# Performance work log

Hardware: AMD Instinct MI355X
Metric: run time of the kernel (lower is better)

The kernel has to match this reference:

```python
import math
import jax, jax.numpy as jnp
import numpy as np

N_EXPERTS = 8
CAPACITY_FACTOR = 1.25
AUX_COEF = 0.01  # forward passes aux_loss_coef to BOTH z-loss and lb-loss


def setup_inputs() -> dict:
    key = jax.random.key(0)
    k1, k2 = jax.random.split(key)
    B, T, D = 4, 4096, 2048
    x = jax.random.normal(k1, (B, T, D), dtype=jnp.float32)
    # nn.Linear(d_model, n_experts, bias=False) weight: (n_experts, d_model)
    W = jax.random.normal(k2, (N_EXPERTS, D), dtype=jnp.float32) * (1.0 / math.sqrt(D))
    return {"x": x, "W": W}


def reference(x, W):
    B, T, D = x.shape
    S = B * T
    E = W.shape[0]
    capacity = int(math.ceil(S / E * CAPACITY_FACTOR))  # static

    x_flat = x.reshape(S, D)
    logits = jnp.einsum("sd,ed->se", x_flat, W)          # (S, E)
    probs = jax.nn.softmax(logits, axis=-1)               # (S, E)
    gate_vals = jnp.max(probs, axis=-1)                   # (S,)
    expert_idx = jnp.argmax(probs, axis=-1)               # (S,) int

    # rank of each token within its expert's queue (token order), 0-based
    onehot = jax.nn.one_hot(expert_idx, E, dtype=jnp.int32)        # (S, E)
    rank = jnp.sum(jnp.cumsum(onehot, axis=0) * onehot, axis=-1) - 1  # (S,)
    keep = rank < capacity
    kept_gates = jnp.where(keep, gate_vals, jnp.zeros((), gate_vals.dtype))

    # z-loss: coef * mean(logsumexp(logits)^2)
    log_z = jax.scipy.special.logsumexp(logits, axis=-1)
    z_loss = AUX_COEF * jnp.mean(log_z * log_z)

    # load-balance loss: coef * E * sum(f_i * p_i)
    p = jnp.mean(probs, axis=0)                                     # (E,)
    counts = jnp.zeros((E,), dtype=probs.dtype).at[expert_idx].add(1.0)
    f = counts / S
    lb_loss = AUX_COEF * E * jnp.sum(f * p)

    aux_loss = z_loss + lb_loss
    return expert_idx, kept_gates, aux_loss
```

## Files before the change

### kernel.cpp

```cpp
#include <hip/hip_runtime.h>

#define S_TOKENS 16384
#define DMODEL   2048
#define NE       8
#define CAPACITY 2560


__global__ __launch_bounds__(512) void logits_kernel(
    const float* __restrict__ x, const float* __restrict__ W,
    int* __restrict__ idx_out, float* __restrict__ gate_out,
    float* __restrict__ partials) {
    __shared__ float Ws[NE][DMODEL];
    __shared__ float sacc[16];

    const int tid  = threadIdx.x;
    const int wave = tid >> 6;
    const int lane = tid & 63;

    if (tid < 16) sacc[tid] = 0.0f;
    {
        const float4* __restrict__ Wg = (const float4*)W;
        float4* Wl = (float4*)Ws;
        #pragma unroll
        for (int i = 0; i < 8; ++i) Wl[i*512 + tid] = Wg[i*512 + tid];
    }
    __syncthreads();

    const int token0 = blockIdx.x * 32 + wave * 4;
    const float4* __restrict__ x0 = (const float4*)(x + (size_t)token0 * DMODEL);
    const float4* __restrict__ x1 = x0 + 512;
    const float4* __restrict__ x2 = x0 + 1024;
    const float4* __restrict__ x3 = x0 + 1536;

    float a0[NE], a1[NE], a2[NE], a3[NE];
    #pragma unroll
    for (int e = 0; e < NE; ++e) { a0[e]=0; a1[e]=0; a2[e]=0; a3[e]=0; }

    #pragma unroll
    for (int i = 0; i < 8; ++i) {
        const int j4 = i*64 + lane;
        float4 xv0 = x0[j4];
        float4 xv1 = x1[j4];
        float4 xv2 = x2[j4];
        float4 xv3 = x3[j4];
        #pragma unroll
        for (int e = 0; e < NE; ++e) {
            float4 w = ((const float4*)Ws[e])[j4];
            a0[e] += xv0.x*w.x + xv0.y*w.y + xv0.z*w.z + xv0.w*w.w;
            a1[e] += xv1.x*w.x + xv1.y*w.y + xv1.z*w.z + xv1.w*w.w;
            a2[e] += xv2.x*w.x + xv2.y*w.y + xv2.z*w.z + xv2.w*w.w;
            a3[e] += xv3.x*w.x + xv3.y*w.y + xv3.z*w.z + xv3.w*w.w;
        }
    }

    const bool hiHalf = (lane & 32) != 0;
    const bool oddQ   = (lane & 16) != 0;
    float lg[NE];
    #pragma unroll
    for (int e = 0; e < NE; ++e) {
        float s0 = a0[e] + __shfl_xor(a0[e], 32);
        float s1 = a1[e] + __shfl_xor(a1[e], 32);
        float s2 = a2[e] + __shfl_xor(a2[e], 32);
        float s3 = a3[e] + __shfl_xor(a3[e], 32);
        float u = hiHalf ? s2 : s0;
        float v = hiHalf ? s3 : s1;
        u += __shfl_xor(u, 16);
        v += __shfl_xor(v, 16);
        float r = oddQ ? v : u;
        r += __shfl_xor(r, 8);
        r += __shfl_xor(r, 4);
        r += __shfl_xor(r, 2);
        r += __shfl_xor(r, 1);
        lg[e] = r;
    }

    const int token = token0 + (lane >> 4);
    const int sub   = lane & 15;

    float m = lg[0]; int e = 0;
    #pragma unroll
    for (int k = 1; k < NE; ++k) { if (lg[k] > m) { m = lg[k]; e = k; } }
    float z = 0.0f;
    #pragma unroll
    for (int k = 0; k < NE; ++k) z += expf(lg[k] - m);
    float gate = 1.0f / z;
    float lz   = m + logf(z);

    if (sub == 0) {
        idx_out[token]  = e;
        gate_out[token] = gate;
        atomicAdd(&sacc[8], lz * lz);
    }
    if (sub < NE) {
        float b0 = (sub & 1) ? lg[1] : lg[0];
        float b1 = (sub & 1) ? lg[3] : lg[2];
        float b2 = (sub & 1) ? lg[5] : lg[4];
        float b3 = (sub & 1) ? lg[7] : lg[6];
        float c0 = (sub & 2) ? b1 : b0;
        float c1 = (sub & 2) ? b3 : b2;
        float ae = (sub & 4) ? c1 : c0;
        atomicAdd(&sacc[sub], expf(ae - m) * gate);
    }

    __syncthreads();
    if (tid < 9) partials[tid*512 + blockIdx.x] = sacc[tid];
}

__global__ __launch_bounds__(512, 1) void finalize_kernel(
    const int* __restrict__ idx, const float* __restrict__ gate,
    const float* __restrict__ partials, float* __restrict__ out) {
    __shared__ float facc[9];
    __shared__ int   cnt[256][9];
    const int t    = threadIdx.x;
    const int wv   = t >> 6;
    const int lane = t & 63;

    if (t < 9) facc[t] = 0.0f;
    __syncthreads();

    #pragma unroll
    for (int q = 0; q < 9; ++q) {
        float v = partials[q*512 + t];
        #pragma unroll
        for (int off = 32; off > 0; off >>= 1) v += __shfl_xor(v, off);
        if (lane == 0) atomicAdd(&facc[q], v);
    }

    const int spanBeg = wv * 32, spanEnd = spanBeg + 32;
    {
        int e = idx[spanBeg*64 + lane];
        for (int s = spanBeg; s < spanEnd; ++s) {
            int en = (s+1 < spanEnd) ? idx[(s+1)*64 + lane] : 0;
            #pragma unroll
            for (int q = 0; q < NE; ++q) {
                unsigned long long mk = __ballot(e == q);
                if (lane == q) cnt[s][q] = (int)__popcll(mk);
            }
            e = en;
        }
    }
    __syncthreads();

    int myc[NE];
    if (t < 256) {
        #pragma unroll
        for (int q = 0; q < NE; ++q) myc[q] = cnt[t][q];
    }
    for (int off = 1; off < 256; off <<= 1) {
        int v[NE];
        if (t < 256) {
            #pragma unroll
            for (int q = 0; q < NE; ++q) v[q] = (t >= off) ? cnt[t-off][q] : 0;
        }
        __syncthreads();
        if (t < 256) {
            #pragma unroll
            for (int q = 0; q < NE; ++q) cnt[t][q] += v[q];
        }
        __syncthreads();
    }

    if (t == 0) {
        float lb = 0.0f;
        #pragma unroll
        for (int q = 0; q < NE; ++q) {
            float f = (float)cnt[255][q] * (1.0f/S_TOKENS);
            float p = facc[q] * (1.0f/S_TOKENS);
            lb += f * p;
        }
        out[2*S_TOKENS] = 0.01f * (facc[8] * (1.0f/S_TOKENS)) + 0.08f * lb;
    }
    __syncthreads();
    if (t < 256) {
        #pragma unroll
        for (int q = 0; q < NE; ++q) cnt[t][q] -= myc[q];
    }
    __syncthreads();

    {
        int   e = idx[spanBeg*64 + lane];
        float g = gate[spanBeg*64 + lane];
        for (int s = spanBeg; s < spanEnd; ++s) {
            int   en = (s+1 < spanEnd) ? idx[(s+1)*64 + lane]  : 0;
            float gn = (s+1 < spanEnd) ? gate[(s+1)*64 + lane] : 0.0f;
            unsigned long long mym = 0;
            #pragma unroll
            for (int q = 0; q < NE; ++q) {
                unsigned long long mk = __ballot(e == q);
                if (e == q) mym = mk;
            }
            unsigned long long lt = (1ull << lane) - 1ull;
            int rank = cnt[s][e] + (int)__popcll(mym & lt);
            int token = s*64 + lane;
            out[token] = (float)e;
            out[S_TOKENS + token] = (rank < CAPACITY) ? g : 0.0f;
            e = en; g = gn;
        }
    }
}

extern "C" void kernel_launch(void* const* d_in, const int* in_sizes, int n_in,
                              void* d_out, int out_size, void* d_ws, size_t ws_size,
                              hipStream_t stream) {
    const float* x = (const float*)d_in[0];
    const float* W = (const float*)d_in[1];
    float* out = (float*)d_out;

    int*   ws_idx  = (int*)d_ws;
    float* ws_gate = (float*)d_ws + 16384;
    float* ws_part = (float*)d_ws + 32768;

    logits_kernel<<<512, 512, 0, stream>>>(x, W, ws_idx, ws_gate, ws_part);
    finalize_kernel<<<1, 512, 0, stream>>>(ws_idx, ws_gate, ws_part, out);
}
```

Measured before the change: 235.5 us.

## Split single-block finalize into scan kernel and parallel per-block output kernel

The single-block finalize, which both built per-chunk expert counts and wrote every token's output serially, is split in two. A 1024-thread scan kernel now computes the exclusive prefix counts per 64-token chunk and the aux loss. A 256-block output kernel then computes ranks and writes outputs in parallel. The logits kernel also changes its main loop from full unroll to unroll 2, to ease register pressure. This adds one extra kernel launch and a global round-trip for the prefix table.

```diff
diff --git a/kernel.cpp b/kernel.cpp
--- a/kernel.cpp
+++ b/kernel.cpp
@@ -10,8 +10,8 @@
     const float* __restrict__ x, const float* __restrict__ W,
     int* __restrict__ idx_out, float* __restrict__ gate_out,
     float* __restrict__ partials) {
-    __shared__ float Ws[NE][DMODEL];
-    __shared__ float sacc[16];
+    __shared__ float4 Ws4[NE][DMODEL/4];
+    __shared__ float  sacc[16];
 
     const int tid  = threadIdx.x;
     const int wave = tid >> 6;
@@ -20,7 +20,7 @@
     if (tid < 16) sacc[tid] = 0.0f;
     {
         const float4* __restrict__ Wg = (const float4*)W;
-        float4* Wl = (float4*)Ws;
+        float4* Wl = (float4*)Ws4;
         #pragma unroll
         for (int i = 0; i < 8; ++i) Wl[i*512 + tid] = Wg[i*512 + tid];
     }
@@ -36,7 +36,7 @@
     #pragma unroll
     for (int e = 0; e < NE; ++e) { a0[e]=0; a1[e]=0; a2[e]=0; a3[e]=0; }
 
-    #pragma unroll
+    #pragma unroll 2
     for (int i = 0; i < 8; ++i) {
         const int j4 = i*64 + lane;
         float4 xv0 = x0[j4];
@@ -45,7 +45,7 @@
         float4 xv3 = x3[j4];
         #pragma unroll
         for (int e = 0; e < NE; ++e) {
-            float4 w = ((const float4*)Ws[e])[j4];
+            float4 w = Ws4[e][j4];
             a0[e] += xv0.x*w.x + xv0.y*w.y + xv0.z*w.z + xv0.w*w.w;
             a1[e] += xv1.x*w.x + xv1.y*w.y + xv1.z*w.z + xv1.w*w.w;
             a2[e] += xv2.x*w.x + xv2.y*w.y + xv2.z*w.z + xv2.w*w.w;
@@ -106,9 +106,9 @@
     if (tid < 9) partials[tid*512 + blockIdx.x] = sacc[tid];
 }
 
-__global__ __launch_bounds__(512, 1) void finalize_kernel(
-    const int* __restrict__ idx, const float* __restrict__ gate,
-    const float* __restrict__ partials, float* __restrict__ out) {
+__global__ __launch_bounds__(1024) void scan_kernel(
+    const int* __restrict__ idx, const float* __restrict__ partials,
+    int* __restrict__ prefix, float* __restrict__ aux_out) {
     __shared__ float facc[9];
     __shared__ int   cnt[256][9];
     const int t    = threadIdx.x;
@@ -118,25 +118,28 @@
     if (t < 9) facc[t] = 0.0f;
     __syncthreads();
 
-    #pragma unroll
-    for (int q = 0; q < 9; ++q) {
-        float v = partials[q*512 + t];
-        #pragma unroll
-        for (int off = 32; off > 0; off >>= 1) v += __shfl_xor(v, off);
-        if (lane == 0) atomicAdd(&facc[q], v);
-    }
-
-    const int spanBeg = wv * 32, spanEnd = spanBeg + 32;
+    if (t < 512) {
+        #pragma unroll
+        for (int q = 0; q < 9; ++q) {
+            float v = partials[q*512 + t];
+            #pragma unroll
+            for (int off = 32; off > 0; off >>= 1) v += __shfl_xor(v, off);
+            if (lane == 0) atomicAdd(&facc[q], v);
+        }
+    }
+
     {
-        int e = idx[spanBeg*64 + lane];
-        for (int s = spanBeg; s < spanEnd; ++s) {
-            int en = (s+1 < spanEnd) ? idx[(s+1)*64 + lane] : 0;
+        const int s0 = wv * 16;
+        int ev[16];
+        #pragma unroll
+        for (int k = 0; k < 16; ++k) ev[k] = idx[(s0+k)*64 + lane];
+        #pragma unroll
+        for (int k = 0; k < 16; ++k) {
             #pragma unroll
             for (int q = 0; q < NE; ++q) {
-                unsigned long long mk = __ballot(e == q);
-                if (lane == q) cnt[s][q] = (int)__popcll(mk);
+                unsigned long long mk = __ballot(ev[k] == q);
+                if (lane == q) cnt[s0+k][q] = (int)__popcll(mk);
             }
-            e = en;
         }
     }
     __syncthreads();
@@ -160,6 +163,10 @@
         __syncthreads();
     }
 
+    if (t < 256) {
+        #pragma unroll
+        for (int q = 0; q < NE; ++q) prefix[t*8 + q] = cnt[t][q] - myc[q];
+    }
     if (t == 0) {
         float lb = 0.0f;
         #pragma unroll
@@ -168,35 +175,30 @@
             float p = facc[q] * (1.0f/S_TOKENS);
             lb += f * p;
         }
-        out[2*S_TOKENS] = 0.01f * (facc[8] * (1.0f/S_TOKENS)) + 0.08f * lb;
-    }
-    __syncthreads();
-    if (t < 256) {
-        #pragma unroll
-        for (int q = 0; q < NE; ++q) cnt[t][q] -= myc[q];
-    }
-    __syncthreads();
-
-    {
-        int   e = idx[spanBeg*64 + lane];
-        float g = gate[spanBeg*64 + lane];
-        for (int s = spanBeg; s < spanEnd; ++s) {
-            int   en = (s+1 < spanEnd) ? idx[(s+1)*64 + lane]  : 0;
-            float gn = (s+1 < spanEnd) ? gate[(s+1)*64 + lane] : 0.0f;
-            unsigned long long mym = 0;
-            #pragma unroll
-            for (int q = 0; q < NE; ++q) {
-                unsigned long long mk = __ballot(e == q);
-                if (e == q) mym = mk;
-            }
-            unsigned long long lt = (1ull << lane) - 1ull;
-            int rank = cnt[s][e] + (int)__popcll(mym & lt);
-            int token = s*64 + lane;
-            out[token] = (float)e;
-            out[S_TOKENS + token] = (rank < CAPACITY) ? g : 0.0f;
-            e = en; g = gn;
-        }
-    }
+        aux_out[0] = 0.01f * (facc[8] * (1.0f/S_TOKENS)) + 0.08f * lb;
+    }
+}
+
+__global__ __launch_bounds__(64) void output_kernel(
+    const int* __restrict__ idx, const float* __restrict__ gate,
+    const int* __restrict__ prefix, float* __restrict__ out) {
+    const int b = blockIdx.x;
+    const int l = threadIdx.x;
+    const int token = b*64 + l;
+    const int e = idx[token];
+    const float g = gate[token];
+
+    unsigned long long mymask = 0;
+    #pragma unroll
+    for (int q = 0; q < NE; ++q) {
+        unsigned long long mk = __ballot(e == q);
+        if (e == q) mymask = mk;
+    }
+    unsigned long long lt = (1ull << l) - 1ull;
+    int rank = prefix[b*8 + e] + (int)__popcll(mymask & lt);
+
+    out[token] = (float)e;
+    out[S_TOKENS + token] = (rank < CAPACITY) ? g : 0.0f;
 }
 
 extern "C" void kernel_launch(void* const* d_in, const int* in_sizes, int n_in,
@@ -206,10 +208,12 @@
     const float* W = (const float*)d_in[1];
     float* out = (float*)d_out;
 
-    int*   ws_idx  = (int*)d_ws;
-    float* ws_gate = (float*)d_ws + 16384;
-    float* ws_part = (float*)d_ws + 32768;
+    int*   ws_idx    = (int*)d_ws;
+    float* ws_gate   = (float*)d_ws + 16384;
+    float* ws_part   = (float*)d_ws + 32768;
+    int*   ws_prefix = (int*)d_ws + 37376;
 
     logits_kernel<<<512, 512, 0, stream>>>(x, W, ws_idx, ws_gate, ws_part);
-    finalize_kernel<<<1, 512, 0, stream>>>(ws_idx, ws_gate, ws_part, out);
-}
+    scan_kernel<<<1, 1024, 0, stream>>>(ws_idx, ws_part, ws_prefix, out + 2*S_TOKENS);
+    output_kernel<<<256, 64, 0, stream>>>(ws_idx, ws_gate, ws_prefix, out);
+}
```

Result: faster. 211.0 us, median of 2 (-10.4%).
